# Optimization experiments

Measured on AMD Instinct MI355X. Metric: run time of the kernel, lower is better.

Reference implementation:

```python
import jax, jax.numpy as jnp
import numpy as np

N_HEADS = 16
D_EMBED = 1024
N_CROSS = 768
D_HEAD = D_EMBED // N_HEADS


def setup_inputs() -> dict:
    key = jax.random.key(0)
    ks = jax.random.split(key, 10)
    B, S = 2, 2048
    x = jax.random.normal(ks[0], (B, S, D_EMBED), dtype=jnp.float32)
    context = jax.random.normal(ks[1], (B, S, N_CROSS), dtype=jnp.float32)
    sq = 1.0 / np.sqrt(D_EMBED)
    sc = 1.0 / np.sqrt(N_CROSS)
    Wq = jax.random.normal(ks[2], (D_EMBED, D_EMBED), dtype=jnp.float32) * sq
    bq = jnp.zeros((D_EMBED,), dtype=jnp.float32)
    Wk = jax.random.normal(ks[3], (N_CROSS, D_EMBED), dtype=jnp.float32) * sc
    bk = jnp.zeros((D_EMBED,), dtype=jnp.float32)
    Wv = jax.random.normal(ks[4], (N_CROSS, D_EMBED), dtype=jnp.float32) * sc
    bv = jnp.zeros((D_EMBED,), dtype=jnp.float32)
    Wo = jax.random.normal(ks[5], (D_EMBED, D_EMBED), dtype=jnp.float32) * sq
    bo = jnp.zeros((D_EMBED,), dtype=jnp.float32)
    return {"x": x, "context": context, "Wq": Wq, "bq": bq, "Wk": Wk, "bk": bk,
            "Wv": Wv, "bv": bv, "Wo": Wo, "bo": bo}


def reference(x, context, Wq, bq, Wk, bk, Wv, bv, Wo, bo):
    B, S, _ = x.shape

    def split_heads(t):  # [B,S,E] -> [B,H,S,Dh]
        return t.reshape(B, S, N_HEADS, D_HEAD).transpose(0, 2, 1, 3)

    q = split_heads(x @ Wq + bq)
    k = split_heads(context @ Wk + bk)
    v = split_heads(context @ Wv + bv)

    scale = 1.0 / np.sqrt(D_HEAD)
    scores = jnp.einsum('bhqd,bhkd->bhqk', q, k) * scale
    attn = jax.nn.softmax(scores, axis=-1)
    out = jnp.einsum('bhqk,bhkd->bhqd', attn, v)
    out = out.transpose(0, 2, 1, 3).reshape(B, S, D_EMBED)
    return out @ Wo + bo
```

## Files before the change

### kernel.cpp

```cpp
#include <hip/hip_runtime.h>
#include <math.h>


namespace {

typedef short bfr __attribute__((ext_vector_type(8)));
typedef short s4v __attribute__((ext_vector_type(4)));
typedef unsigned u4v __attribute__((ext_vector_type(4)));
typedef float accf __attribute__((ext_vector_type(16)));

#define MFMA32(a, b, c) __builtin_amdgcn_mfma_f32_32x32x16_bf16(a, b, c, 0, 0, 0)

__device__ inline short f2bf(float f) {
    unsigned u = __float_as_uint(f);
    u += 0x7fffu + ((u >> 16) & 1u);
    return (short)(u >> 16);
}
__device__ inline float fexp2(float x) { return __builtin_amdgcn_exp2f(x); }
__device__ inline accf zero16() {
    accf z;
#pragma unroll
    for (int i = 0; i < 16; ++i) z[i] = 0.f;
    return z;
}
__device__ inline void dma16(const void* g, void* l) {
    __builtin_amdgcn_global_load_lds(
        (const __attribute__((address_space(1))) void*)g,
        (__attribute__((address_space(3))) void*)l, 16, 0, 0);
}

__global__ __launch_bounds__(256) void tobf2(const float* __restrict__ x,
                                             const float* __restrict__ c,
                                             short* __restrict__ xb,
                                             short* __restrict__ cb) {
    int i = blockIdx.x * 256 + threadIdx.x;
    if (i < 1048576) {
        float4 v = ((const float4*)x)[i];
        s4v p = {f2bf(v.x), f2bf(v.y), f2bf(v.z), f2bf(v.w)};
        ((s4v*)xb)[i] = p;
    } else {
        int j = i - 1048576;
        float4 v = ((const float4*)c)[j];
        s4v p = {f2bf(v.x), f2bf(v.y), f2bf(v.z), f2bf(v.w)};
        ((s4v*)cb)[j] = p;
    }
}

__global__ __launch_bounds__(256) void wtrans4(
    const float* __restrict__ Wq, const float* __restrict__ Wk,
    const float* __restrict__ Wv, const float* __restrict__ Wo,
    short* __restrict__ Wqt, short* __restrict__ Wkt,
    short* __restrict__ Wvt, short* __restrict__ Wot) {
    const float* W;
    short* Wt;
    int K;
    switch (blockIdx.z) {
        case 0: W = Wq; Wt = Wqt; K = 1024; break;
        case 1: W = Wk; Wt = Wkt; K = 768; break;
        case 2: W = Wv; Wt = Wvt; K = 768; break;
        default: W = Wo; Wt = Wot; K = 1024; break;
    }
    const int k0 = blockIdx.y * 64;
    if (k0 >= K) return;
    __shared__ short t[64][68];
    const int tid = threadIdx.x;
    const int n0 = blockIdx.x * 64;
    const int kr = tid >> 4, nc = (tid & 15) * 4;
#pragma unroll
    for (int rep = 0; rep < 4; ++rep) {
        int k = kr + rep * 16;
        float4 v = *(const float4*)&W[(size_t)(k0 + k) * 1024 + n0 + nc];
        t[nc + 0][k] = f2bf(v.x);
        t[nc + 1][k] = f2bf(v.y);
        t[nc + 2][k] = f2bf(v.z);
        t[nc + 3][k] = f2bf(v.w);
    }
    __syncthreads();
    const int nr = tid >> 4, kc = (tid & 15) * 4;
#pragma unroll
    for (int rep = 0; rep < 4; ++rep) {
        int n = nr + rep * 16;
        s4v p = {t[n][kc], t[n][kc + 1], t[n][kc + 2], t[n][kc + 3]};
        *(s4v*)&Wt[(size_t)(n0 + n) * K + k0 + kc] = p;
    }
}

__global__ __launch_bounds__(256) void gemm_qkv(
    const short* __restrict__ xb, const short* __restrict__ cb,
    const short* __restrict__ Wqt, const short* __restrict__ Wkt,
    const short* __restrict__ Wvt, const float* __restrict__ bq,
    const float* __restrict__ bk, const float* __restrict__ bv,
    short* __restrict__ Qf, short* __restrict__ Kf, short* __restrict__ Vt,
    float qscale) {
    const int z = blockIdx.z;
    const short* A  = (z == 0) ? xb : cb;
    const short* Bt = (z == 0) ? Wqt : ((z == 1) ? Wkt : Wvt);
    const float* bias = (z == 0) ? bq : ((z == 1) ? bk : bv);
    const int K = (z == 0) ? 1024 : 768;
    const float scale = (z == 0) ? qscale : 1.f;
    short* out = (z == 0) ? Qf : ((z == 1) ? Kf : Vt);

    __shared__ short As[4096];
    __shared__ short Bs[4096];
    const int t = threadIdx.x, lane = t & 63, w = t >> 6;
    const int lm = lane & 31, h2 = lane >> 5;
    const int wm = w & 1, wn = w >> 1;
    const int m0 = blockIdx.y * 128, n0 = blockIdx.x * 128;

    const int srow = t >> 2, scol = (t & 3) * 8;
    const short* ga = A + (size_t)(m0 + srow) * K + scol;
    const short* gb = Bt + (size_t)(n0 + srow) * K + scol;
    short* lA = As + w * 512;
    short* lB = Bs + w * 512;

    const int aoff = (wm * 64 + lm) * 32 + h2 * 8;
    const int boff = (wn * 64 + lm) * 32 + h2 * 8;

    accf acc[2][2] = {zero16(), zero16(), zero16(), zero16()};

    for (int kt = 0; kt < K; kt += 32) {
        __syncthreads();
        dma16(ga + kt, lA);
        dma16(ga + (size_t)64 * K + kt, lA + 2048);
        dma16(gb + kt, lB);
        dma16(gb + (size_t)64 * K + kt, lB + 2048);
        __syncthreads();
#pragma unroll
        for (int kk = 0; kk < 32; kk += 16) {
            bfr a0 = *(const bfr*)&As[aoff + kk];
            bfr a1 = *(const bfr*)&As[aoff + 1024 + kk];
            bfr b0 = *(const bfr*)&Bs[boff + kk];
            bfr b1 = *(const bfr*)&Bs[boff + 1024 + kk];
            acc[0][0] = MFMA32(a0, b0, acc[0][0]);
            acc[0][1] = MFMA32(a0, b1, acc[0][1]);
            acc[1][0] = MFMA32(a1, b0, acc[1][0]);
            acc[1][1] = MFMA32(a1, b1, acc[1][1]);
        }
    }

#pragma unroll
    for (int nt = 0; nt < 2; ++nt) {
        const int n = n0 + wn * 64 + nt * 32 + lm;
        const float bn = bias[n];
        const int hh = n >> 6, dd = n & 63;
#pragma unroll
        for (int mt = 0; mt < 2; ++mt) {
            const int mbase = m0 + wm * 64 + mt * 32 + 4 * h2;
            if (z != 2) {
                const int cb2 = (dd >> 4) * 512 + ((dd >> 3) & 1) * 256 + (dd & 7);
#pragma unroll
                for (int r = 0; r < 16; ++r) {
                    const int m = mbase + (r & 3) + 8 * (r >> 2);
                    const int bb = m >> 11, q = m & 2047;
                    float v = (acc[mt][nt][r] + bn) * scale;
                    out[((size_t)((bb * 16 + hh) * 64 + (q >> 5))) * 2048 +
                        cb2 + (q & 31) * 8] = f2bf(v);
                }
            } else {
                const int dblk = dd >> 5, lmv = dd & 31;
#pragma unroll
                for (int g = 0; g < 4; ++g) {
                    const int m = mbase + 8 * g;
                    const int bb = m >> 11, s = m & 2047;
                    const int kvt = s >> 6, kc = (s >> 4) & 3;
                    const int h2v = (s >> 3) & 1, j0 = s & 7;
                    s4v p = {f2bf(acc[mt][nt][4 * g + 0] + bn),
                             f2bf(acc[mt][nt][4 * g + 1] + bn),
                             f2bf(acc[mt][nt][4 * g + 2] + bn),
                             f2bf(acc[mt][nt][4 * g + 3] + bn)};
                    *(s4v*)(out +
                            ((size_t)(((bb * 16 + hh) * 32 + kvt) * 2 + dblk)) * 2048 +
                            kc * 512 + h2v * 256 + lmv * 8 + j0) = p;
                }
            }
        }
    }
}

__global__ __launch_bounds__(256) void gemm_out(
    const short* __restrict__ A, const short* __restrict__ Bt,
    const float* __restrict__ bias, float* __restrict__ out, int K) {
    __shared__ short As[4096];
    __shared__ short Bs[4096];
    const int t = threadIdx.x, lane = t & 63, w = t >> 6;
    const int lm = lane & 31, h2 = lane >> 5;
    const int wm = w & 1, wn = w >> 1;
    const int m0 = blockIdx.y * 128, n0 = blockIdx.x * 128;

    const int srow = t >> 2, scol = (t & 3) * 8;
    const short* ga = A + (size_t)(m0 + srow) * K + scol;
    const short* gb = Bt + (size_t)(n0 + srow) * K + scol;
    short* lA = As + w * 512;
    short* lB = Bs + w * 512;

    const int aoff = (wm * 64 + lm) * 32 + h2 * 8;
    const int boff = (wn * 64 + lm) * 32 + h2 * 8;

    accf acc[2][2] = {zero16(), zero16(), zero16(), zero16()};

    for (int kt = 0; kt < K; kt += 32) {
        __syncthreads();
        dma16(ga + kt, lA);
        dma16(ga + (size_t)64 * K + kt, lA + 2048);
        dma16(gb + kt, lB);
        dma16(gb + (size_t)64 * K + kt, lB + 2048);
        __syncthreads();
#pragma unroll
        for (int kk = 0; kk < 32; kk += 16) {
            bfr a0 = *(const bfr*)&As[aoff + kk];
            bfr a1 = *(const bfr*)&As[aoff + 1024 + kk];
            bfr b0 = *(const bfr*)&Bs[boff + kk];
            bfr b1 = *(const bfr*)&Bs[boff + 1024 + kk];
            acc[0][0] = MFMA32(a0, b0, acc[0][0]);
            acc[0][1] = MFMA32(a0, b1, acc[0][1]);
            acc[1][0] = MFMA32(a1, b0, acc[1][0]);
            acc[1][1] = MFMA32(a1, b1, acc[1][1]);
        }
    }

#pragma unroll
    for (int nt = 0; nt < 2; ++nt) {
        const int n = n0 + wn * 64 + nt * 32 + lm;
        const float bn = bias[n];
#pragma unroll
        for (int mt = 0; mt < 2; ++mt) {
            const int mbase = m0 + wm * 64 + mt * 32 + 4 * h2;
#pragma unroll
            for (int r = 0; r < 16; ++r) {
                const int m = mbase + (r & 3) + 8 * (r >> 2);
                out[(size_t)m * 1024 + n] = acc[mt][nt][r] + bn;
            }
        }
    }
}

__global__ __launch_bounds__(256) void attn(
    const short* __restrict__ Qf, const short* __restrict__ Kf,
    const short* __restrict__ Vt, short* __restrict__ ao) {
    __shared__ short smem[16384];
    const int bid = blockIdx.x;
    const int hidx = bid & 31, qb = bid >> 5;
    const int b = hidx >> 4, h = hidx & 15;
    const int lane = threadIdx.x & 63, wv = threadIdx.x >> 6;
    const int lm = lane & 31, h2 = lane >> 5;
    const bool hb = h2 != 0;
    const int q0 = qb * 128 + wv * 32;

    const short* qbase =
        Qf + ((size_t)(hidx * 64 + (q0 >> 5))) * 2048 + lane * 8;
    bfr qf[4];
#pragma unroll
    for (int kc = 0; kc < 4; ++kc) qf[kc] = *(const bfr*)(qbase + kc * 512);

    const short* khead = Kf + (size_t)hidx * 131072;
    const short* vhead = Vt + (size_t)hidx * 131072;
    const short* gsrc =
        ((wv < 2) ? (khead + wv * 2048) : (vhead + (wv - 2) * 2048)) + lane * 8;

#pragma unroll
    for (int i = 0; i < 4; ++i)
        dma16(gsrc + i * 512, &smem[wv * 2048 + i * 512]);

    accf oa0 = zero16(), oa1 = zero16();
    float la0 = 0.f, la1 = 0.f, la2 = 0.f, la3 = 0.f;

#pragma unroll 1
    for (int it = 0; it < 32; ++it) {
        const int p = it & 1;
        __syncthreads();
        if (it + 1 < 32) {
            const short* gn = gsrc + (size_t)(it + 1) * 4096;
            short* ln = &smem[(1 - p) * 8192 + wv * 2048];
#pragma unroll
            for (int i = 0; i < 4; ++i) dma16(gn + i * 512, ln + i * 512);
        }
        const short* kb = &smem[p * 8192];
        bfr kf0[4], kf1[4], vf0[4], vf1[4];
#pragma unroll
        for (int kc = 0; kc < 4; ++kc) {
            kf0[kc] = *(const bfr*)&kb[kc * 512 + lane * 8];
            kf1[kc] = *(const bfr*)&kb[2048 + kc * 512 + lane * 8];
            vf0[kc] = *(const bfr*)&kb[4096 + kc * 512 + lane * 8];
            vf1[kc] = *(const bfr*)&kb[6144 + kc * 512 + lane * 8];
        }
        accf s0 = zero16(), s1 = zero16();
#pragma unroll
        for (int kc = 0; kc < 4; ++kc) {
            s0 = MFMA32(kf0[kc], qf[kc], s0);
            s1 = MFMA32(kf1[kc], qf[kc], s1);
        }

#pragma unroll
        for (int i = 0; i < 16; ++i) s0[i] = fexp2(s0[i]);
#pragma unroll
        for (int i = 0; i < 16; ++i) s1[i] = fexp2(s1[i]);
#pragma unroll
        for (int i = 0; i < 16; ++i) {
            if ((i & 3) == 0) la0 += s0[i] + s1[i];
            else if ((i & 3) == 1) la1 += s0[i] + s1[i];
            else if ((i & 3) == 2) la2 += s0[i] + s1[i];
            else la3 += s0[i] + s1[i];
        }

        bfr pb[4];
#pragma unroll
        for (int kc = 0; kc < 4; ++kc) {
            const int base = 8 * (kc & 1);
            float e[8];
#pragma unroll
            for (int i = 0; i < 4; ++i) {
                float lo = (kc < 2) ? s0[base + i] : s1[base + i];
                float hi = (kc < 2) ? s0[base + 4 + i] : s1[base + 4 + i];
                float own = hb ? hi : lo;
                float con = hb ? lo : hi;
                float rcv = __shfl_xor(con, 32);
                e[i]     = hb ? rcv : own;
                e[4 + i] = hb ? own : rcv;
            }
            u4v pw;
#pragma unroll
            for (int j = 0; j < 4; ++j)
                pw[j] = __builtin_amdgcn_perm(__float_as_uint(e[2 * j + 1]),
                                              __float_as_uint(e[2 * j]),
                                              0x07060302u);
            pb[kc] = __builtin_bit_cast(bfr, pw);
        }

#pragma unroll
        for (int kc = 0; kc < 4; ++kc) {
            oa0 = MFMA32(vf0[kc], pb[kc], oa0);
            oa1 = MFMA32(vf1[kc], pb[kc], oa1);
        }
    }

    float ls = la0 + la1 + la2 + la3;
    ls += __shfl_xor(ls, 32);
    const float inv = 1.f / ls;

    short* orow = ao + (size_t)(b * 2048 + q0 + lm) * 1024 + h * 64;
#pragma unroll
    for (int dt = 0; dt < 2; ++dt) {
        const accf& oa = dt ? oa1 : oa0;
#pragma unroll
        for (int g = 0; g < 4; ++g) {
            const int d0 = dt * 32 + 4 * h2 + 8 * g;
            s4v p = {f2bf(oa[4 * g + 0] * inv), f2bf(oa[4 * g + 1] * inv),
                     f2bf(oa[4 * g + 2] * inv), f2bf(oa[4 * g + 3] * inv)};
            *(s4v*)(orow + d0) = p;
        }
    }
}

}

extern "C" void kernel_launch(void* const* d_in, const int* in_sizes, int n_in,
                              void* d_out, int out_size, void* d_ws,
                              size_t ws_size, hipStream_t stream) {
    const float* x   = (const float*)d_in[0];
    const float* ctx = (const float*)d_in[1];
    const float* Wq  = (const float*)d_in[2];
    const float* bq  = (const float*)d_in[3];
    const float* Wk  = (const float*)d_in[4];
    const float* bk  = (const float*)d_in[5];
    const float* Wv  = (const float*)d_in[6];
    const float* bv  = (const float*)d_in[7];
    const float* Wo  = (const float*)d_in[8];
    const float* bo  = (const float*)d_in[9];

    short* xb  = (short*)d_ws;
    short* cb  = xb + (size_t)4096 * 1024;
    short* Wqt = cb + (size_t)4096 * 768;
    short* Wkt = Wqt + (size_t)1024 * 1024;
    short* Wvt = Wkt + (size_t)1024 * 768;
    short* Wot = Wvt + (size_t)1024 * 768;
    short* Qf  = Wot + (size_t)1024 * 1024;
    short* Kf  = Qf + (size_t)4096 * 1024;
    short* Vt  = Kf + (size_t)4096 * 1024;

    tobf2<<<7168, 256, 0, stream>>>(x, ctx, xb, cb);
    wtrans4<<<dim3(16, 16, 4), 256, 0, stream>>>(Wq, Wk, Wv, Wo,
                                                 Wqt, Wkt, Wvt, Wot);

    const float qscale = 0.125f * 1.44269504088896f;
    gemm_qkv<<<dim3(8, 32, 3), 256, 0, stream>>>(xb, cb, Wqt, Wkt, Wvt,
                                                 bq, bk, bv, Qf, Kf, Vt,
                                                 qscale);

    attn<<<512, 256, 0, stream>>>(Qf, Kf, Vt, xb);

    gemm_out<<<dim3(8, 32), 256, 0, stream>>>(xb, Wot, bo, (float*)d_out, 1024);
}
```

Measured before the change: 227.2 us.

## Split attention over KV halves with combine pass; fuse prep kernels; widen gemm_out

Attention now splits each head's 2048 keys into two halves, doubling the block count to 1024. Each block writes unnormalised bf16 partial outputs plus per-row exp-sums, and a new combine kernel adds the partials and normalises. The aim is more parallelism and occupancy, with a launch bound of 3 blocks per CU. This costs an extra pass over two 8MB partial buffers and some precision from bf16 partials. The change also merges the two prep kernels into one launch, gives gemm_out 512 threads with a smaller per-wave tile, and packs P to bf16 before the cross-lane shuffle so fewer values are exchanged.

```diff
diff --git a/kernel.cpp b/kernel.cpp
--- a/kernel.cpp
+++ b/kernel.cpp
@@ -16,6 +16,9 @@
     u += 0x7fffu + ((u >> 16) & 1u);
     return (short)(u >> 16);
 }
+__device__ inline float bf2f(short s) {
+    return __uint_as_float(((unsigned)(unsigned short)s) << 16);
+}
 __device__ inline float fexp2(float x) { return __builtin_amdgcn_exp2f(x); }
 __device__ inline accf zero16() {
     accf z;
@@ -29,42 +32,44 @@
         (__attribute__((address_space(3))) void*)l, 16, 0, 0);
 }
 
-__global__ __launch_bounds__(256) void tobf2(const float* __restrict__ x,
-                                             const float* __restrict__ c,
-                                             short* __restrict__ xb,
-                                             short* __restrict__ cb) {
-    int i = blockIdx.x * 256 + threadIdx.x;
-    if (i < 1048576) {
-        float4 v = ((const float4*)x)[i];
-        s4v p = {f2bf(v.x), f2bf(v.y), f2bf(v.z), f2bf(v.w)};
-        ((s4v*)xb)[i] = p;
-    } else {
-        int j = i - 1048576;
-        float4 v = ((const float4*)c)[j];
-        s4v p = {f2bf(v.x), f2bf(v.y), f2bf(v.z), f2bf(v.w)};
-        ((s4v*)cb)[j] = p;
-    }
-}
-
-__global__ __launch_bounds__(256) void wtrans4(
+__global__ __launch_bounds__(256) void prep(
+    const float* __restrict__ x, const float* __restrict__ ctx,
+    short* __restrict__ xb, short* __restrict__ cb,
     const float* __restrict__ Wq, const float* __restrict__ Wk,
     const float* __restrict__ Wv, const float* __restrict__ Wo,
     short* __restrict__ Wqt, short* __restrict__ Wkt,
     short* __restrict__ Wvt, short* __restrict__ Wot) {
+    __shared__ short t[64][68];
+    const int bx = blockIdx.x;
+    if (bx < 7168) {
+        int i = bx * 256 + threadIdx.x;
+        if (i < 1048576) {
+            float4 v = ((const float4*)x)[i];
+            s4v p = {f2bf(v.x), f2bf(v.y), f2bf(v.z), f2bf(v.w)};
+            ((s4v*)xb)[i] = p;
+        } else {
+            int j = i - 1048576;
+            float4 v = ((const float4*)ctx)[j];
+            s4v p = {f2bf(v.x), f2bf(v.y), f2bf(v.z), f2bf(v.w)};
+            ((s4v*)cb)[j] = p;
+        }
+        return;
+    }
+    const int idx = bx - 7168;
+    const int z = idx >> 8, gy = (idx >> 4) & 15, gx = idx & 15;
     const float* W;
     short* Wt;
     int K;
-    switch (blockIdx.z) {
+    switch (z) {
         case 0: W = Wq; Wt = Wqt; K = 1024; break;
         case 1: W = Wk; Wt = Wkt; K = 768; break;
         case 2: W = Wv; Wt = Wvt; K = 768; break;
         default: W = Wo; Wt = Wot; K = 1024; break;
     }
-    const int k0 = blockIdx.y * 64;
+    const int k0 = gy * 64;
     if (k0 >= K) return;
-    __shared__ short t[64][68];
     const int tid = threadIdx.x;
-    const int n0 = blockIdx.x * 64;
+    const int n0 = gx * 64;
     const int kr = tid >> 4, nc = (tid & 15) * 4;
 #pragma unroll
     for (int rep = 0; rep < 4; ++rep) {
@@ -177,7 +182,7 @@
     }
 }
 
-__global__ __launch_bounds__(256) void gemm_out(
+__global__ __launch_bounds__(512) void gemm_out(
     const short* __restrict__ A, const short* __restrict__ Bt,
     const float* __restrict__ bias, float* __restrict__ out, int K) {
     __shared__ short As[4096];
@@ -194,52 +199,46 @@
     short* lB = Bs + w * 512;
 
     const int aoff = (wm * 64 + lm) * 32 + h2 * 8;
-    const int boff = (wn * 64 + lm) * 32 + h2 * 8;
-
-    accf acc[2][2] = {zero16(), zero16(), zero16(), zero16()};
+    const int boff = (wn * 32 + lm) * 32 + h2 * 8;
+
+    accf acc[2] = {zero16(), zero16()};
 
     for (int kt = 0; kt < K; kt += 32) {
         __syncthreads();
         dma16(ga + kt, lA);
-        dma16(ga + (size_t)64 * K + kt, lA + 2048);
         dma16(gb + kt, lB);
-        dma16(gb + (size_t)64 * K + kt, lB + 2048);
         __syncthreads();
 #pragma unroll
         for (int kk = 0; kk < 32; kk += 16) {
             bfr a0 = *(const bfr*)&As[aoff + kk];
             bfr a1 = *(const bfr*)&As[aoff + 1024 + kk];
             bfr b0 = *(const bfr*)&Bs[boff + kk];
-            bfr b1 = *(const bfr*)&Bs[boff + 1024 + kk];
-            acc[0][0] = MFMA32(a0, b0, acc[0][0]);
-            acc[0][1] = MFMA32(a0, b1, acc[0][1]);
-            acc[1][0] = MFMA32(a1, b0, acc[1][0]);
-            acc[1][1] = MFMA32(a1, b1, acc[1][1]);
-        }
-    }
-
-#pragma unroll
-    for (int nt = 0; nt < 2; ++nt) {
-        const int n = n0 + wn * 64 + nt * 32 + lm;
-        const float bn = bias[n];
-#pragma unroll
-        for (int mt = 0; mt < 2; ++mt) {
-            const int mbase = m0 + wm * 64 + mt * 32 + 4 * h2;
-#pragma unroll
-            for (int r = 0; r < 16; ++r) {
-                const int m = mbase + (r & 3) + 8 * (r >> 2);
-                out[(size_t)m * 1024 + n] = acc[mt][nt][r] + bn;
-            }
-        }
-    }
-}
-
-__global__ __launch_bounds__(256) void attn(
+            acc[0] = MFMA32(a0, b0, acc[0]);
+            acc[1] = MFMA32(a1, b0, acc[1]);
+        }
+    }
+
+    const int n = n0 + wn * 32 + lm;
+    const float bn = bias[n];
+#pragma unroll
+    for (int mt = 0; mt < 2; ++mt) {
+        const int mbase = m0 + wm * 64 + mt * 32 + 4 * h2;
+#pragma unroll
+        for (int r = 0; r < 16; ++r) {
+            const int m = mbase + (r & 3) + 8 * (r >> 2);
+            out[(size_t)m * 1024 + n] = acc[mt][r] + bn;
+        }
+    }
+}
+
+__global__ __launch_bounds__(256, 3) void attn(
     const short* __restrict__ Qf, const short* __restrict__ Kf,
-    const short* __restrict__ Vt, short* __restrict__ ao) {
+    const short* __restrict__ Vt, short* __restrict__ part,
+    float* __restrict__ lsum) {
     __shared__ short smem[16384];
     const int bid = blockIdx.x;
-    const int hidx = bid & 31, qb = bid >> 5;
+    const int hidx = bid & 31, qs = bid >> 5;
+    const int split = qs & 1, qb = qs >> 1;
     const int b = hidx >> 4, h = hidx & 15;
     const int lane = threadIdx.x & 63, wv = threadIdx.x >> 6;
     const int lm = lane & 31, h2 = lane >> 5;
@@ -252,8 +251,8 @@
 #pragma unroll
     for (int kc = 0; kc < 4; ++kc) qf[kc] = *(const bfr*)(qbase + kc * 512);
 
-    const short* khead = Kf + (size_t)hidx * 131072;
-    const short* vhead = Vt + (size_t)hidx * 131072;
+    const short* khead = Kf + (size_t)hidx * 131072 + split * 65536;
+    const short* vhead = Vt + (size_t)hidx * 131072 + split * 65536;
     const short* gsrc =
         ((wv < 2) ? (khead + wv * 2048) : (vhead + (wv - 2) * 2048)) + lane * 8;
 
@@ -262,13 +261,13 @@
         dma16(gsrc + i * 512, &smem[wv * 2048 + i * 512]);
 
     accf oa0 = zero16(), oa1 = zero16();
-    float la0 = 0.f, la1 = 0.f, la2 = 0.f, la3 = 0.f;
+    float la0 = 0.f, la1 = 0.f;
 
 #pragma unroll 1
-    for (int it = 0; it < 32; ++it) {
+    for (int it = 0; it < 16; ++it) {
         const int p = it & 1;
         __syncthreads();
-        if (it + 1 < 32) {
+        if (it + 1 < 16) {
             const short* gn = gsrc + (size_t)(it + 1) * 4096;
             short* ln = &smem[(1 - p) * 8192 + wv * 2048];
 #pragma unroll
@@ -296,33 +295,33 @@
         for (int i = 0; i < 16; ++i) s1[i] = fexp2(s1[i]);
 #pragma unroll
         for (int i = 0; i < 16; ++i) {
-            if ((i & 3) == 0) la0 += s0[i] + s1[i];
-            else if ((i & 3) == 1) la1 += s0[i] + s1[i];
-            else if ((i & 3) == 2) la2 += s0[i] + s1[i];
-            else la3 += s0[i] + s1[i];
+            if (i & 1) la1 += s0[i] + s1[i];
+            else       la0 += s0[i] + s1[i];
         }
 
         bfr pb[4];
 #pragma unroll
         for (int kc = 0; kc < 4; ++kc) {
+            const accf& s = (kc < 2) ? s0 : s1;
             const int base = 8 * (kc & 1);
-            float e[8];
-#pragma unroll
-            for (int i = 0; i < 4; ++i) {
-                float lo = (kc < 2) ? s0[base + i] : s1[base + i];
-                float hi = (kc < 2) ? s0[base + 4 + i] : s1[base + 4 + i];
-                float own = hb ? hi : lo;
-                float con = hb ? lo : hi;
-                float rcv = __shfl_xor(con, 32);
-                e[i]     = hb ? rcv : own;
-                e[4 + i] = hb ? own : rcv;
-            }
-            u4v pw;
-#pragma unroll
-            for (int j = 0; j < 4; ++j)
-                pw[j] = __builtin_amdgcn_perm(__float_as_uint(e[2 * j + 1]),
-                                              __float_as_uint(e[2 * j]),
-                                              0x07060302u);
+            unsigned Lw0 = __builtin_amdgcn_perm(__float_as_uint(s[base + 1]),
+                                                 __float_as_uint(s[base + 0]),
+                                                 0x07060302u);
+            unsigned Lw1 = __builtin_amdgcn_perm(__float_as_uint(s[base + 3]),
+                                                 __float_as_uint(s[base + 2]),
+                                                 0x07060302u);
+            unsigned Hw0 = __builtin_amdgcn_perm(__float_as_uint(s[base + 5]),
+                                                 __float_as_uint(s[base + 4]),
+                                                 0x07060302u);
+            unsigned Hw1 = __builtin_amdgcn_perm(__float_as_uint(s[base + 7]),
+                                                 __float_as_uint(s[base + 6]),
+                                                 0x07060302u);
+            unsigned c0 = hb ? Lw0 : Hw0;
+            unsigned c1 = hb ? Lw1 : Hw1;
+            unsigned r0 = (unsigned)__shfl_xor((int)c0, 32);
+            unsigned r1 = (unsigned)__shfl_xor((int)c1, 32);
+            u4v pw = {hb ? r0 : Lw0, hb ? r1 : Lw1,
+                      hb ? Hw0 : r0, hb ? Hw1 : r1};
             pb[kc] = __builtin_bit_cast(bfr, pw);
         }
 
@@ -333,22 +332,42 @@
         }
     }
 
-    float ls = la0 + la1 + la2 + la3;
+    float ls = la0 + la1;
     ls += __shfl_xor(ls, 32);
-    const float inv = 1.f / ls;
-
-    short* orow = ao + (size_t)(b * 2048 + q0 + lm) * 1024 + h * 64;
+    if (!hb) lsum[((size_t)(split * 2 + b) * 16 + h) * 2048 + q0 + lm] = ls;
+
+    short* orow = part + (size_t)split * 4194304 +
+                  (size_t)(b * 2048 + q0 + lm) * 1024 + h * 64;
 #pragma unroll
     for (int dt = 0; dt < 2; ++dt) {
         const accf& oa = dt ? oa1 : oa0;
 #pragma unroll
         for (int g = 0; g < 4; ++g) {
             const int d0 = dt * 32 + 4 * h2 + 8 * g;
-            s4v p = {f2bf(oa[4 * g + 0] * inv), f2bf(oa[4 * g + 1] * inv),
-                     f2bf(oa[4 * g + 2] * inv), f2bf(oa[4 * g + 3] * inv)};
+            s4v p = {f2bf(oa[4 * g + 0]), f2bf(oa[4 * g + 1]),
+                     f2bf(oa[4 * g + 2]), f2bf(oa[4 * g + 3])};
             *(s4v*)(orow + d0) = p;
         }
     }
+}
+
+__global__ __launch_bounds__(256) void combine(
+    const short* __restrict__ p0, const short* __restrict__ p1,
+    const float* __restrict__ lsum, short* __restrict__ ao) {
+    const int t = blockIdx.x * 256 + threadIdx.x;
+    const int col8 = t & 127, m = t >> 7;
+    const int h = col8 >> 3;
+    const int b = m >> 11, q = m & 2047;
+    const float l0 = lsum[((size_t)(0 + b) * 16 + h) * 2048 + q];
+    const float l1 = lsum[((size_t)(2 + b) * 16 + h) * 2048 + q];
+    const float inv = 1.f / (l0 + l1);
+    const size_t e0 = (size_t)m * 1024 + col8 * 8;
+    bfr a = *(const bfr*)(p0 + e0);
+    bfr c = *(const bfr*)(p1 + e0);
+    bfr r;
+#pragma unroll
+    for (int j = 0; j < 8; ++j) r[j] = f2bf((bf2f(a[j]) + bf2f(c[j])) * inv);
+    *(bfr*)(ao + e0) = r;
 }
 
 }
@@ -376,17 +395,20 @@
     short* Qf  = Wot + (size_t)1024 * 1024;
     short* Kf  = Qf + (size_t)4096 * 1024;
     short* Vt  = Kf + (size_t)4096 * 1024;
-
-    tobf2<<<7168, 256, 0, stream>>>(x, ctx, xb, cb);
-    wtrans4<<<dim3(16, 16, 4), 256, 0, stream>>>(Wq, Wk, Wv, Wo,
-                                                 Wqt, Wkt, Wvt, Wot);
+    short* p0  = Vt + (size_t)4096 * 1024;
+    short* p1  = p0 + (size_t)4096 * 1024;
+    float* lsum = (float*)(p1 + (size_t)4096 * 1024);
+
+    prep<<<8192, 256, 0, stream>>>(x, ctx, xb, cb, Wq, Wk, Wv, Wo,
+                                   Wqt, Wkt, Wvt, Wot);
 
     const float qscale = 0.125f * 1.44269504088896f;
     gemm_qkv<<<dim3(8, 32, 3), 256, 0, stream>>>(xb, cb, Wqt, Wkt, Wvt,
                                                  bq, bk, bv, Qf, Kf, Vt,
                                                  qscale);
 
-    attn<<<512, 256, 0, stream>>>(Qf, Kf, Vt, xb);
-
-    gemm_out<<<dim3(8, 32), 256, 0, stream>>>(xb, Wot, bo, (float*)d_out, 1024);
-}
+    attn<<<1024, 256, 0, stream>>>(Qf, Kf, Vt, p0, lsum);
+    combine<<<2048, 256, 0, stream>>>(p0, p1, lsum, xb);
+
+    gemm_out<<<dim3(8, 32), 512, 0, stream>>>(xb, Wot, bo, (float*)d_out, 1024);
+}
```

Result: no change. 222.9 us (-1.9%).
